# Kernel optimization log

Hardware: AMD Instinct MI355X
Metric: run time of the kernel (lower is better)

## Reference

```python
import jax, jax.numpy as jnp
import numpy as np

EPS = 1e-6
B, N, M, C, H = 4, 2048, 1024, 1024, 16
HD = C // H          # 64
HID = 4 * C          # 4096
SCALE = 1.0 / np.sqrt(HD)


def _ln(x, g, b):
    m = x.mean(-1, keepdims=True)
    v = jnp.mean((x - m) ** 2, -1, keepdims=True)
    return (x - m) * jax.lax.rsqrt(v + EPS) * g + b


def _rot(x):
    # interleaved rotate: (-x2, x1) pairs (rotate_half=False path)
    x1, x2 = x[..., ::2], x[..., 1::2]
    return jnp.stack([-x2, x1], axis=-1).reshape(x.shape)


def _apply_rope(x, emb):
    # emb: [N, 2*HD] = cat(sin, cos); x: [B,H,N,HD]
    sin, cos = jnp.split(emb, 2, axis=-1)
    return x * cos + _rot(x) * sin


def _sdpa(q, k, v):
    s = jnp.einsum('bhqd,bhkd->bhqk', q, k) * SCALE
    a = jax.nn.softmax(s, axis=-1)
    return jnp.einsum('bhqk,bhkd->bhqd', a, v)


def _forward(x, ctx, rope,
             wqkv, sa_qg, sa_qb, sa_kg, sa_kb, sa_wo, sa_bo,
             ca_wq, ca_wk, ca_wv, ca_qg, ca_qb, ca_kg, ca_kb, ca_wo, ca_bo, ca_gate,
             w1g, b1g, w1x, b1x, w2, b2, ls0, ls1, ls2):
    Bx, Nx, Cx = x.shape
    Mx = ctx.shape[1]
    # ---- self attention (fused QKV, qk-norm, RoPE) ----
    qkv = (x @ wqkv).reshape(Bx, Nx, 3, H, HD).transpose(2, 0, 3, 1, 4)  # [3,B,H,N,HD]
    q, k, v = qkv[0], qkv[1], qkv[2]
    q = _ln(q, sa_qg, sa_qb)
    k = _ln(k, sa_kg, sa_kb)
    q = _apply_rope(q, rope)
    k = _apply_rope(k, rope)
    sa = _sdpa(q, k, v).transpose(0, 2, 1, 3).reshape(Bx, Nx, Cx)
    sa = sa @ sa_wo + sa_bo
    x = ls0 * sa + x
    # ---- cross attention (GQA degenerate: n_kv_heads == n_q_heads), gated ----
    q = (x @ ca_wq).reshape(Bx, Nx, H, HD).transpose(0, 2, 1, 3)
    k = (ctx @ ca_wk).reshape(Bx, Mx, H, HD).transpose(0, 2, 1, 3)
    v = (ctx @ ca_wv).reshape(Bx, Mx, H, HD).transpose(0, 2, 1, 3)
    q = _ln(q, ca_qg, ca_qb)
    k = _ln(k, ca_kg, ca_kb)
    q = _apply_rope(q, rope)  # rope on queries only; ctx has its own positions
    ca = _sdpa(q, k, v).transpose(0, 2, 1, 3).reshape(Bx, Nx, Cx)
    ca = (ca @ ca_wo + ca_bo) * jnp.tanh(ca_gate)
    x = ls1 * ca + x
    # ---- SwiGLU FFN ----
    h = jax.nn.silu(x @ w1g + b1g) * (x @ w1x + b1x)
    f = h @ w2 + b2
    x = ls2 * f + x
    return x


def setup_inputs() -> dict:
    key = jax.random.key(0)
    ks = iter(jax.random.split(key, 32))
    rn = lambda shape, s=0.02: (jax.random.normal(next(ks), shape, jnp.float32) * s)
    inp = {
        'x': jax.random.normal(next(ks), (B, N, C), jnp.float32),
        'ctx': jax.random.normal(next(ks), (B, M, C), jnp.float32),
    }
    # rotary table: cat(sin, cos), interleaved-repeated freqs -> [N, 2*HD]
    pos = jnp.arange(N, dtype=jnp.float32)
    inv = 1.0 / (10000.0 ** (jnp.arange(0, HD, 2, dtype=jnp.float32) / HD))
    ang = pos[:, None] * inv[None, :]                      # [N, HD/2]
    sin = jnp.repeat(jnp.sin(ang), 2, axis=-1)
    cos = jnp.repeat(jnp.cos(ang), 2, axis=-1)
    inp['rope'] = jnp.concatenate([sin, cos], axis=-1)
    inp.update(
        wqkv=rn((C, 3 * C)),
        sa_qg=jnp.ones((HD,)), sa_qb=jnp.zeros((HD,)),
        sa_kg=jnp.ones((HD,)), sa_kb=jnp.zeros((HD,)),
        sa_wo=rn((C, C)), sa_bo=jnp.zeros((C,)),
        ca_wq=rn((C, C)), ca_wk=rn((C, C)), ca_wv=rn((C, C)),
        ca_qg=jnp.ones((HD,)), ca_qb=jnp.zeros((HD,)),
        ca_kg=jnp.ones((HD,)), ca_kb=jnp.zeros((HD,)),
        ca_wo=rn((C, C)), ca_bo=jnp.zeros((C,)),
        ca_gate=jnp.full((C,), 0.5, jnp.float32),
        w1g=rn((C, HID)), b1g=jnp.zeros((HID,)),
        w1x=rn((C, HID)), b1x=jnp.zeros((HID,)),
        w2=rn((HID, C)), b2=jnp.zeros((C,)),
        ls0=jnp.full((C,), 1e-5, jnp.float32),
        ls1=jnp.full((C,), 1e-5, jnp.float32),
        ls2=jnp.full((C,), 1e-5, jnp.float32),
    )
    return inp


def reference(x, ctx, rope,
              wqkv, sa_qg, sa_qb, sa_kg, sa_kb, sa_wo, sa_bo,
              ca_wq, ca_wk, ca_wv, ca_qg, ca_qb, ca_kg, ca_kb, ca_wo, ca_bo, ca_gate,
              w1g, b1g, w1x, b1x, w2, b2, ls0, ls1, ls2):
    return _forward(x, ctx, rope,
                    wqkv, sa_qg, sa_qb, sa_kg, sa_kb, sa_wo, sa_bo,
                    ca_wq, ca_wk, ca_wv, ca_qg, ca_qb, ca_kg, ca_kb, ca_wo, ca_bo, ca_gate,
                    w1g, b1g, w1x, b1x, w2, b2, ls0, ls1, ls2)
```

## Files before the change

kernel.cpp:

```cpp
#include <hip/hip_runtime.h>
#include <hip/hip_bf16.h>
#include <math.h>


typedef __attribute__((ext_vector_type(8))) short bf16x8;
typedef __attribute__((ext_vector_type(4))) short s16x4;
typedef __attribute__((ext_vector_type(4))) float f32x4;

#define DEV __device__ __forceinline__

DEV unsigned short f2us(float f) {
  __hip_bfloat16 h = __float2bfloat16(f);
  return __builtin_bit_cast(unsigned short, h);
}

DEV void gload_lds16(const void* g, void* l) {
  __builtin_amdgcn_global_load_lds((const __attribute__((address_space(1))) void*)g,
                                   (__attribute__((address_space(3))) void*)l, 16, 0, 0);
}

#define MFMA_BF16_16x16x32 __builtin_amdgcn_mfma_f32_16x16x32_bf16
#define WAITV0 asm volatile("s_waitcnt vmcnt(0)" ::: "memory")


__global__ __launch_bounds__(256) void cvt_f32_bf16(const float* __restrict__ in,
                                                    __hip_bfloat16* __restrict__ out,
                                                    long n) {
  long i = ((long)blockIdx.x * blockDim.x + threadIdx.x) * 4;
  if (i + 3 < n) {
    float4 v = *(const float4*)(in + i);
    out[i + 0] = __float2bfloat16(v.x);
    out[i + 1] = __float2bfloat16(v.y);
    out[i + 2] = __float2bfloat16(v.z);
    out[i + 3] = __float2bfloat16(v.w);
  }
}

__global__ __launch_bounds__(256) void transpose_cvt(const float* __restrict__ w,
                                                     __hip_bfloat16* __restrict__ wT,
                                                     int K, int N) {
  __shared__ float tile[32][33];
  int n0 = blockIdx.x * 32, k0 = blockIdx.y * 32;
  int tx = threadIdx.x, ty = threadIdx.y;
  #pragma unroll
  for (int i = 0; i < 32; i += 8)
    tile[ty + i][tx] = w[(long)(k0 + ty + i) * N + n0 + tx];
  __syncthreads();
  #pragma unroll
  for (int i = 0; i < 32; i += 8)
    wT[(long)(n0 + ty + i) * K + k0 + tx] = __float2bfloat16(tile[tx][ty + i]);
}

__global__ __launch_bounds__(256) void transpose_cvt_ilv(const float* __restrict__ w,
                                                         __hip_bfloat16* __restrict__ wI,
                                                         int K, int N, int ofs) {
  __shared__ float tile[32][33];
  int n0 = blockIdx.x * 32, k0 = blockIdx.y * 32;
  int tx = threadIdx.x, ty = threadIdx.y;
  #pragma unroll
  for (int i = 0; i < 32; i += 8)
    tile[ty + i][tx] = w[(long)(k0 + ty + i) * N + n0 + tx];
  __syncthreads();
  #pragma unroll
  for (int i = 0; i < 32; i += 8) {
    int j = n0 + ty + i;
    int r = 32 * (j >> 4) + (j & 15) + ofs;
    wI[(long)r * K + k0 + tx] = __float2bfloat16(tile[tx][ty + i]);
  }
}

__global__ __launch_bounds__(256) void transpose_v(const __hip_bfloat16* __restrict__ v,
                                                   long vBatch, long vRow,
                                                   __hip_bfloat16* __restrict__ vt,
                                                   int Nkv) {
  __shared__ unsigned short tile[32][36];
  int bh = blockIdx.z;
  int b = bh >> 4, h = bh & 15;
  int kv0 = blockIdx.x * 32;
  int d0 = blockIdx.y * 32;
  int tx = threadIdx.x, ty = threadIdx.y;
  const __hip_bfloat16* src = v + (long)b * vBatch + h * 64 + d0;
  #pragma unroll
  for (int i = 0; i < 32; i += 8)
    tile[ty + i][tx] = __builtin_bit_cast(unsigned short, src[(long)(kv0 + ty + i) * vRow + tx]);
  __syncthreads();
  unsigned short* dst = (unsigned short*)vt + ((long)bh * (Nkv >> 6) + (kv0 >> 6)) * 4608 + (kv0 & 32) + tx;
  #pragma unroll
  for (int i = 0; i < 32; i += 8)
    dst[(long)(d0 + ty + i) * 72] = tile[tx][ty + i];
}

__global__ __launch_bounds__(256) void ln_rope(__hip_bfloat16* __restrict__ buf,
                                               const float* __restrict__ rope,
                                               const float* __restrict__ g0,
                                               const float* __restrict__ b0,
                                               const float* __restrict__ g1,
                                               const float* __restrict__ b1,
                                               int Rows, int W,
                                               long rowStride, long whichStride,
                                               int ropeMask, long total) {
  int lane = threadIdx.x & 63;
  int wv = threadIdx.x >> 6;
  long id = (long)blockIdx.x * 4 + wv;
  if (id >= total) return;
  int which = (int)(id % W);
  long t = id / W;
  int h = (int)(t & 15); t >>= 4;
  int n = (int)(t % Rows);
  int b = (int)(t / Rows);
  __hip_bfloat16* p = buf + ((long)b * Rows + n) * rowStride + (long)which * whichStride + h * 64 + lane;
  float v = __bfloat162float(*p);
  float s = v;
  #pragma unroll
  for (int m = 32; m; m >>= 1) s += __shfl_xor(s, m);
  float mean = s * (1.f / 64.f);
  float d = v - mean;
  float q = d * d;
  #pragma unroll
  for (int m = 32; m; m >>= 1) q += __shfl_xor(q, m);
  float rstd = rsqrtf(q * (1.f / 64.f) + 1e-6f);
  const float* g = which ? g1 : g0;
  const float* bb = which ? b1 : b0;
  float xn = d * rstd * g[lane] + bb[lane];
  if ((ropeMask >> which) & 1) {
    float partner = __shfl_xor(xn, 1);
    float sn = rope[(long)n * 128 + lane];
    float cs = rope[(long)n * 128 + 64 + lane];
    xn = (lane & 1) ? (xn * cs + partner * sn) : (xn * cs - partner * sn);
  }
  *p = __float2bfloat16(xn);
}

template <int EPI>
DEV void epi_store(long idx, long col, float v,
                   float* __restrict__ out_f, __hip_bfloat16* __restrict__ out_b,
                   const float* __restrict__ bias, const float* __restrict__ scale,
                   const float* __restrict__ gate, const float* __restrict__ resid,
                   const __hip_bfloat16* __restrict__ mulin) {
  if constexpr (EPI == 0) {
    out_b[idx] = __float2bfloat16(v);
  } else if constexpr (EPI == 1) {
    float r = scale[col] * (v + bias[col]) + resid[idx];
    out_f[idx] = r;
    out_b[idx] = __float2bfloat16(r);
  } else if constexpr (EPI == 2) {
    float r = scale[col] * ((v + bias[col]) * tanhf(gate[col])) + resid[idx];
    out_f[idx] = r;
    out_b[idx] = __float2bfloat16(r);
  } else if constexpr (EPI == 3) {
    float z = v + bias[col];
    out_b[idx] = __float2bfloat16(z / (1.f + expf(-z)));
  } else if constexpr (EPI == 4) {
    float z = (v + bias[col]) * __bfloat162float(mulin[idx]);
    out_b[idx] = __float2bfloat16(z);
  } else {
    out_f[idx] = scale[col] * (v + bias[col]) + resid[idx];
  }
}

template <int EPI>
__global__ __launch_bounds__(256) void gemm128(const __hip_bfloat16* __restrict__ A,
                                               const __hip_bfloat16* __restrict__ Bt,
                                               int M, int N, int K,
                                               float* __restrict__ out_f,
                                               __hip_bfloat16* __restrict__ out_b,
                                               const float* __restrict__ bias,
                                               const float* __restrict__ scale,
                                               const float* __restrict__ gate,
                                               const float* __restrict__ resid,
                                               const __hip_bfloat16* __restrict__ mulin) {
  __shared__ unsigned short As[128 * 32];
  __shared__ unsigned short Bs[128 * 32];
  int t = threadIdx.x;
  int l = t & 63;
  int w = t >> 6;
  int wr = w >> 1, wc = w & 1;
  long bm = blockIdx.x, bn = blockIdx.y;
  const __hip_bfloat16* Ab = A + bm * 128 * (long)K;
  const __hip_bfloat16* Bb = Bt + bn * 128 * (long)K;

  f32x4 acc[4][4] = {};

  for (int k0 = 0; k0 < K; k0 += 32) {
    #pragma unroll
    for (int j = 0; j < 2; j++) {
      int c = j * 256 + t;
      int row = c >> 2;
      int ko = (c & 3) * 8;
      gload_lds16(Ab + (long)row * K + k0 + ko, &As[c * 8]);
      gload_lds16(Bb + (long)row * K + k0 + ko, &Bs[c * 8]);
    }
    __syncthreads();
    bf16x8 af[4], bfg[4];
    #pragma unroll
    for (int m = 0; m < 4; m++)
      af[m] = *(const bf16x8*)&As[(wr * 64 + m * 16 + (l & 15)) * 32 + (l >> 4) * 8];
    #pragma unroll
    for (int n = 0; n < 4; n++)
      bfg[n] = *(const bf16x8*)&Bs[(wc * 64 + n * 16 + (l & 15)) * 32 + (l >> 4) * 8];
    #pragma unroll
    for (int m = 0; m < 4; m++)
      #pragma unroll
      for (int n = 0; n < 4; n++)
        acc[m][n] = MFMA_BF16_16x16x32(af[m], bfg[n], acc[m][n], 0, 0, 0);
    __syncthreads();
  }

  #pragma unroll
  for (int m = 0; m < 4; m++)
    #pragma unroll
    for (int n = 0; n < 4; n++)
      #pragma unroll
      for (int i = 0; i < 4; i++) {
        long row = bm * 128 + wr * 64 + m * 16 + (l >> 4) * 4 + i;
        long col = bn * 128 + wc * 64 + n * 16 + (l & 15);
        epi_store<EPI>(row * (long)N + col, col, acc[m][n][i],
                       out_f, out_b, bias, scale, gate, resid, mulin);
      }
}

template <int BM, int EPI>
__global__ __launch_bounds__(512, 2) void gemm2ph(const __hip_bfloat16* __restrict__ A,
                                                  const __hip_bfloat16* __restrict__ Bt,
                                                  int M, int N, int K,
                                                  float* __restrict__ out_f,
                                                  __hip_bfloat16* __restrict__ out_b,
                                                  const float* __restrict__ bias,
                                                  const float* __restrict__ scale,
                                                  const float* __restrict__ gate,
                                                  const float* __restrict__ resid,
                                                  const __hip_bfloat16* __restrict__ mulin) {
  constexpr int MF = BM / 32;
  constexpr int WRS = BM / 2;
  constexpr int AJ = BM * 8 / 512;
  __shared__ __align__(16) unsigned short As[2][BM * 64];
  __shared__ __align__(16) unsigned short Bs[2][256 * 64];

  int t = threadIdx.x;
  int l = t & 63, w = t >> 6;
  int lo = l & 15, hi = l >> 4;
  int wr = w >> 2, wc = w & 3;
  long bm = blockIdx.x, bn = blockIdx.y;
  const __hip_bfloat16* Ab = A + bm * BM * (long)K;
  const __hip_bfloat16* Bb = Bt + bn * 256 * (long)K;
  int nt = K >> 6;

  auto stage = [&](int kt, int buf) {
    long kb = (long)kt * 64;
    #pragma unroll
    for (int j = 0; j < AJ; j++) {
      int q = j * 512 + t;
      int row = q >> 3, c = (q & 7) ^ (row & 7);
      gload_lds16(Ab + (long)row * K + kb + c * 8, &As[buf][q * 8]);
    }
    #pragma unroll
    for (int j = 0; j < 4; j++) {
      int q = j * 512 + t;
      int row = q >> 3, c = (q & 7) ^ (row & 7);
      gload_lds16(Bb + (long)row * K + kb + c * 8, &Bs[buf][q * 8]);
    }
  };

  f32x4 acc[MF][4] = {};

  stage(0, 0);
  WAITV0;
  __builtin_amdgcn_s_barrier();

  for (int kt = 0; kt < nt; ++kt) {
    int cur = kt & 1;
    if (kt + 1 < nt) stage(kt + 1, cur ^ 1);

    #pragma unroll
    for (int ks = 0; ks < 2; ks++) {
      bf16x8 bfrag[4];
      #pragma unroll
      for (int n = 0; n < 4; n++) {
        int rb = wc * 64 + n * 16 + lo;
        bfrag[n] = *(const bf16x8*)&Bs[cur][rb * 64 + (((ks << 2) | hi) ^ (rb & 7)) * 8];
      }
      #pragma unroll
      for (int mg = 0; mg < MF; mg += 4) {
        bf16x8 afrag[4];
        #pragma unroll
        for (int m = 0; m < 4; m++) {
          int ra = wr * WRS + (mg + m) * 16 + lo;
          afrag[m] = *(const bf16x8*)&As[cur][ra * 64 + (((ks << 2) | hi) ^ (ra & 7)) * 8];
        }
        __builtin_amdgcn_s_setprio(1);
        #pragma unroll
        for (int m = 0; m < 4; m++)
          #pragma unroll
          for (int n = 0; n < 4; n++)
            acc[mg + m][n] = MFMA_BF16_16x16x32(afrag[m], bfrag[n], acc[mg + m][n], 0, 0, 0);
        __builtin_amdgcn_s_setprio(0);
      }
    }

    if (kt + 1 < nt) {
      WAITV0;
      __builtin_amdgcn_s_barrier();
    }
  }

  if constexpr (EPI == 6) {
    #pragma unroll
    for (int m = 0; m < MF; m++)
      #pragma unroll
      for (int np = 0; np < 2; np++)
        #pragma unroll
        for (int i = 0; i < 4; i++) {
          long row = bm * BM + wr * WRS + m * 16 + hi * 4 + i;
          long jc = bn * 128 + wc * 32 + np * 16 + lo;
          float g = acc[m][np * 2][i] + bias[jc];
          float xv = acc[m][np * 2 + 1][i] + gate[jc];
          float hv = (g / (1.f + expf(-g))) * xv;
          out_b[row * (long)(N >> 1) + jc] = __float2bfloat16(hv);
        }
  } else {
    #pragma unroll
    for (int m = 0; m < MF; m++)
      #pragma unroll
      for (int n = 0; n < 4; n++)
        #pragma unroll
        for (int i = 0; i < 4; i++) {
          long row = bm * BM + wr * WRS + m * 16 + hi * 4 + i;
          long col = bn * 256 + wc * 64 + n * 16 + lo;
          epi_store<EPI>(row * (long)N + col, col, acc[m][n][i],
                         out_f, out_b, bias, scale, gate, resid, mulin);
        }
  }
}

__global__ __launch_bounds__(256) void attn32(const __hip_bfloat16* __restrict__ qB, long qBatch, long qRow,
                                              const __hip_bfloat16* __restrict__ kB, long kBatch, long kRow,
                                              const __hip_bfloat16* __restrict__ vt,
                                              __hip_bfloat16* __restrict__ out, int Nq, int Nkv) {
  const float SC2 = 0.125f * 1.44269504089f;
  int t = threadIdx.x;
  int l = t & 63, w = t >> 6;
  int lo = l & 15, hi = l >> 4;
  int nQC = Nq >> 7;
  int qc = blockIdx.x % nQC;
  int bh = blockIdx.x / nQC;
  int h = bh & 15, b = bh >> 4;
  int q0 = qc * 128 + w * 32;

  __shared__ unsigned short P_all[4][32 * 72];
  __shared__ unsigned short V_lds[2][64 * 72];
  unsigned short* P = P_all[w];

  bf16x8 qf[2][2];
#pragma unroll
  for (int qs = 0; qs < 2; qs++) {
    const __hip_bfloat16* qp = qB + (long)b * qBatch + (long)(q0 + qs * 16 + lo) * qRow + h * 64 + hi * 8;
    qf[qs][0] = *(const bf16x8*)qp;
    qf[qs][1] = *(const bf16x8*)(qp + 32);
  }

  float mrow[2] = {-INFINITY, -INFINITY};
  float lsum[2] = {0.f, 0.f};
  f32x4 acc[2][4] = {};
  const f32x4 fz = {0.f, 0.f, 0.f, 0.f};

  const __hip_bfloat16* kbase = kB + (long)b * kBatch + h * 64 + hi * 8;
  int nt = Nkv >> 6;
  const char* vtb = (const char*)vt + (long)bh * nt * 9216;

  auto stageV = [&](int tile, unsigned short* dstb) {
    const char* src = vtb + (long)tile * 9216;
    gload_lds16(src + t * 16, &dstb[t * 8]);
    gload_lds16(src + (t + 256) * 16, &dstb[(t + 256) * 8]);
    if (t < 64) gload_lds16(src + (t + 512) * 16, &dstb[(t + 512) * 8]);
  };
  auto loadK = [&](int tile, bf16x8 (&kg)[4][2]) {
#pragma unroll
    for (int g = 0; g < 4; g++) {
      const __hip_bfloat16* kp = kbase + (long)(tile * 64 + g * 16 + lo) * kRow;
      kg[g][0] = *(const bf16x8*)kp;
      kg[g][1] = *(const bf16x8*)(kp + 32);
    }
  };
  auto qkt = [&](bf16x8 (&kg)[4][2], f32x4 (&ST)[2][4]) {
#pragma unroll
    for (int qs = 0; qs < 2; qs++)
#pragma unroll
      for (int g = 0; g < 4; g++) {
        f32x4 s0 = MFMA_BF16_16x16x32(kg[g][0], qf[qs][0], fz, 0, 0, 0);
        ST[qs][g] = MFMA_BF16_16x16x32(kg[g][1], qf[qs][1], s0, 0, 0, 0);
      }
  };
  auto smax = [&](f32x4 (&ST)[2][4]) {
#pragma unroll
    for (int qs = 0; qs < 2; qs++) {
      float mg0 = fmaxf(fmaxf(ST[qs][0][0], ST[qs][0][1]), fmaxf(ST[qs][0][2], ST[qs][0][3]));
      float mg1 = fmaxf(fmaxf(ST[qs][1][0], ST[qs][1][1]), fmaxf(ST[qs][1][2], ST[qs][1][3]));
      float mg2 = fmaxf(fmaxf(ST[qs][2][0], ST[qs][2][1]), fmaxf(ST[qs][2][2], ST[qs][2][3]));
      float mg3 = fmaxf(fmaxf(ST[qs][3][0], ST[qs][3][1]), fmaxf(ST[qs][3][2], ST[qs][3][3]));
      float rm = fmaxf(fmaxf(mg0, mg1), fmaxf(mg2, mg3)) * SC2;
      rm = fmaxf(rm, __shfl_xor(rm, 16));
      rm = fmaxf(rm, __shfl_xor(rm, 32));
      if (!__all(rm <= mrow[qs] + 8.f)) {
        float mn = fmaxf(mrow[qs], rm);
        float scl = exp2f(mrow[qs] - mn);
        mrow[qs] = mn;
        lsum[qs] *= scl;
        float c0 = __shfl(scl, hi * 4 + 0);
        float c1 = __shfl(scl, hi * 4 + 1);
        float c2 = __shfl(scl, hi * 4 + 2);
        float c3 = __shfl(scl, hi * 4 + 3);
#pragma unroll
        for (int tt = 0; tt < 4; tt++) {
          acc[qs][tt][0] *= c0; acc[qs][tt][1] *= c1;
          acc[qs][tt][2] *= c2; acc[qs][tt][3] *= c3;
        }
      }
      float m = mrow[qs];
      float rs = 0.f;
#pragma unroll
      for (int g = 0; g < 4; g++) {
        float p0 = exp2f(fmaf(ST[qs][g][0], SC2, -m));
        float p1 = exp2f(fmaf(ST[qs][g][1], SC2, -m));
        float p2 = exp2f(fmaf(ST[qs][g][2], SC2, -m));
        float p3 = exp2f(fmaf(ST[qs][g][3], SC2, -m));
        rs += (p0 + p1) + (p2 + p3);
        s16x4 pw;
        pw[0] = (short)f2us(p0); pw[1] = (short)f2us(p1);
        pw[2] = (short)f2us(p2); pw[3] = (short)f2us(p3);
        *(s16x4*)&P[(qs * 16 + lo) * 72 + g * 16 + hi * 4] = pw;
      }
      rs += __shfl_xor(rs, 16);
      rs += __shfl_xor(rs, 32);
      lsum[qs] += rs;
    }
  };
  auto pv = [&](const unsigned short* Vb) {
    bf16x8 pf[2][2];
#pragma unroll
    for (int qs = 0; qs < 2; qs++) {
      pf[qs][0] = *(const bf16x8*)&P[(qs * 16 + lo) * 72 + hi * 8];
      pf[qs][1] = *(const bf16x8*)&P[(qs * 16 + lo) * 72 + 32 + hi * 8];
    }
#pragma unroll
    for (int tt = 0; tt < 4; tt++) {
      bf16x8 v0 = *(const bf16x8*)&Vb[(tt * 16 + lo) * 72 + hi * 8];
      bf16x8 v1 = *(const bf16x8*)&Vb[(tt * 16 + lo) * 72 + 32 + hi * 8];
#pragma unroll
      for (int qs = 0; qs < 2; qs++) {
        acc[qs][tt] = MFMA_BF16_16x16x32(pf[qs][0], v0, acc[qs][tt], 0, 0, 0);
        acc[qs][tt] = MFMA_BF16_16x16x32(pf[qs][1], v1, acc[qs][tt], 0, 0, 0);
      }
    }
  };

  bf16x8 kgA[4][2], kgB[4][2];
  stageV(0, V_lds[0]);
  loadK(0, kgA);

  for (int it = 0; it < nt; it += 2) {
    __syncthreads();
    stageV(it + 1, V_lds[1]);
    f32x4 ST0[2][4];
    qkt(kgA, ST0);
    loadK(it + 1, kgB);
    smax(ST0);
    pv(V_lds[0]);

    __syncthreads();
    if (it + 2 < nt) stageV(it + 2, V_lds[0]);
    f32x4 ST1[2][4];
    qkt(kgB, ST1);
    if (it + 2 < nt) loadK(it + 2, kgA);
    smax(ST1);
    pv(V_lds[1]);
  }

#pragma unroll
  for (int qs = 0; qs < 2; qs++) {
    float inv = 1.f / lsum[qs];
    float iv0 = __shfl(inv, hi * 4 + 0);
    float iv1 = __shfl(inv, hi * 4 + 1);
    float iv2 = __shfl(inv, hi * 4 + 2);
    float iv3 = __shfl(inv, hi * 4 + 3);
    float iv[4] = {iv0, iv1, iv2, iv3};
#pragma unroll
    for (int i = 0; i < 4; i++) {
      long row = q0 + qs * 16 + hi * 4 + i;
      __hip_bfloat16* op = out + ((long)b * Nq + row) * 1024 + h * 64 + lo;
#pragma unroll
      for (int tt = 0; tt < 4; tt++) op[tt * 16] = __float2bfloat16(acc[qs][tt][i] * iv[i]);
    }
  }
}


extern "C" void kernel_launch(void* const* d_in, const int* in_sizes, int n_in,
                              void* d_out, int out_size, void* d_ws, size_t ws_size,
                              hipStream_t stream) {
  (void)in_sizes; (void)n_in; (void)out_size; (void)ws_size;

  const float* x      = (const float*)d_in[0];
  const float* ctx    = (const float*)d_in[1];
  const float* rope   = (const float*)d_in[2];
  const float* wqkv   = (const float*)d_in[3];
  const float* sa_qg  = (const float*)d_in[4];
  const float* sa_qb  = (const float*)d_in[5];
  const float* sa_kg  = (const float*)d_in[6];
  const float* sa_kb  = (const float*)d_in[7];
  const float* sa_wo  = (const float*)d_in[8];
  const float* sa_bo  = (const float*)d_in[9];
  const float* ca_wq  = (const float*)d_in[10];
  const float* ca_wk  = (const float*)d_in[11];
  const float* ca_wv  = (const float*)d_in[12];
  const float* ca_qg  = (const float*)d_in[13];
  const float* ca_qb  = (const float*)d_in[14];
  const float* ca_kg  = (const float*)d_in[15];
  const float* ca_kb  = (const float*)d_in[16];
  const float* ca_wo  = (const float*)d_in[17];
  const float* ca_bo  = (const float*)d_in[18];
  const float* ca_gate= (const float*)d_in[19];
  const float* w1g    = (const float*)d_in[20];
  const float* b1g    = (const float*)d_in[21];
  const float* w1x    = (const float*)d_in[22];
  const float* b1x    = (const float*)d_in[23];
  const float* w2     = (const float*)d_in[24];
  const float* b2     = (const float*)d_in[25];
  const float* ls0    = (const float*)d_in[26];
  const float* ls1    = (const float*)d_in[27];
  const float* ls2    = (const float*)d_in[28];

  char* ws = (char*)d_ws;

  const long OFF_WQKVT = 0;
  const long OFF_SAWOT = 6291456;
  const long OFF_CAWQT = 8388608;
  const long OFF_CAWKT = 10485760;
  const long OFF_CAWVT = 12582912;
  const long OFF_CAWOT = 14680064;
  const long OFF_W1I   = 16777216;
  const long OFF_W2T   = 33554432;
  const long OFF_XB    = 41943040;
  const long OFF_QC    = OFF_XB;
  const long OFF_CTXB  = 58720256;
  const long OFF_QKV   = 67108864;
  const long OFF_CAO   = 67108864;
  const long OFF_X2B   = 83886080;
  const long OFF_SG    = 100663296;
  const long OFF_SAO   = 117440512;
  const long OFF_KC    = 117440512;
  const long OFF_VC    = 125829120;
  const long OFF_X1    = 134217728;
  const long OFF_X1B   = 167772160;
  const long OFF_CAVT  = OFF_X1B;
  const long OFF_X2    = 184549376;
  const long OFF_SAVT  = OFF_X2;

  auto bfp = [&](long off) { return (__hip_bfloat16*)(ws + off); };
  auto ffp = [&](long off) { return (float*)(ws + off); };

  dim3 tb32(32, 8);
  transpose_cvt<<<dim3(96, 32), tb32, 0, stream>>>(wqkv,  bfp(OFF_WQKVT), 1024, 3072);
  transpose_cvt<<<dim3(32, 32), tb32, 0, stream>>>(sa_wo, bfp(OFF_SAWOT), 1024, 1024);
  transpose_cvt<<<dim3(32, 32), tb32, 0, stream>>>(ca_wq, bfp(OFF_CAWQT), 1024, 1024);
  transpose_cvt<<<dim3(32, 32), tb32, 0, stream>>>(ca_wk, bfp(OFF_CAWKT), 1024, 1024);
  transpose_cvt<<<dim3(32, 32), tb32, 0, stream>>>(ca_wv, bfp(OFF_CAWVT), 1024, 1024);
  transpose_cvt<<<dim3(32, 32), tb32, 0, stream>>>(ca_wo, bfp(OFF_CAWOT), 1024, 1024);
  transpose_cvt_ilv<<<dim3(128, 32), tb32, 0, stream>>>(w1g, bfp(OFF_W1I), 1024, 4096, 0);
  transpose_cvt_ilv<<<dim3(128, 32), tb32, 0, stream>>>(w1x, bfp(OFF_W1I), 1024, 4096, 16);
  transpose_cvt<<<dim3(32, 128), tb32, 0, stream>>>(w2,   bfp(OFF_W2T), 4096, 1024);

  cvt_f32_bf16<<<8192, 256, 0, stream>>>(x,   bfp(OFF_XB),   8388608);
  cvt_f32_bf16<<<4096, 256, 0, stream>>>(ctx, bfp(OFF_CTXB), 4194304);

  gemm2ph<256, 0><<<dim3(32, 12), 512, 0, stream>>>(bfp(OFF_XB), bfp(OFF_WQKVT), 8192, 3072, 1024,
                                                    nullptr, bfp(OFF_QKV), nullptr, nullptr, nullptr, nullptr, nullptr);

  transpose_v<<<dim3(64, 2, 64), tb32, 0, stream>>>(bfp(OFF_QKV) + 2048, (long)2048 * 3072, 3072,
                                                    bfp(OFF_SAVT), 2048);

  ln_rope<<<65536, 256, 0, stream>>>(bfp(OFF_QKV), rope, sa_qg, sa_qb, sa_kg, sa_kb,
                                     2048, 2, 3 * 1024, 1024, 3, (long)4 * 2048 * 16 * 2);

  attn32<<<1024, 256, 0, stream>>>(bfp(OFF_QKV),        (long)2048 * 3072, 3072,
                                   bfp(OFF_QKV) + 1024, (long)2048 * 3072, 3072,
                                   bfp(OFF_SAVT), bfp(OFF_SAO), 2048, 2048);

  gemm2ph<128, 1><<<dim3(64, 4), 512, 0, stream>>>(bfp(OFF_SAO), bfp(OFF_SAWOT), 8192, 1024, 1024,
                                                   ffp(OFF_X1), bfp(OFF_X1B), sa_bo, ls0, nullptr, x, nullptr);

  gemm2ph<128, 0><<<dim3(64, 4), 512, 0, stream>>>(bfp(OFF_X1B), bfp(OFF_CAWQT), 8192, 1024, 1024,
                                                   nullptr, bfp(OFF_QC), nullptr, nullptr, nullptr, nullptr, nullptr);
  gemm128<0><<<dim3(32, 8), 256, 0, stream>>>(bfp(OFF_CTXB), bfp(OFF_CAWKT), 4096, 1024, 1024,
                                              nullptr, bfp(OFF_KC), nullptr, nullptr, nullptr, nullptr, nullptr);
  gemm128<0><<<dim3(32, 8), 256, 0, stream>>>(bfp(OFF_CTXB), bfp(OFF_CAWVT), 4096, 1024, 1024,
                                              nullptr, bfp(OFF_VC), nullptr, nullptr, nullptr, nullptr, nullptr);

  transpose_v<<<dim3(32, 2, 64), tb32, 0, stream>>>(bfp(OFF_VC), (long)1024 * 1024, 1024,
                                                    bfp(OFF_CAVT), 1024);

  ln_rope<<<32768, 256, 0, stream>>>(bfp(OFF_QC), rope, ca_qg, ca_qb, ca_qg, ca_qb,
                                     2048, 1, 1024, 0, 1, (long)4 * 2048 * 16);
  ln_rope<<<16384, 256, 0, stream>>>(bfp(OFF_KC), rope, ca_kg, ca_kb, ca_kg, ca_kb,
                                     1024, 1, 1024, 0, 0, (long)4 * 1024 * 16);

  attn32<<<1024, 256, 0, stream>>>(bfp(OFF_QC), (long)2048 * 1024, 1024,
                                   bfp(OFF_KC), (long)1024 * 1024, 1024,
                                   bfp(OFF_CAVT), bfp(OFF_CAO), 2048, 1024);

  gemm2ph<128, 2><<<dim3(64, 4), 512, 0, stream>>>(bfp(OFF_CAO), bfp(OFF_CAWOT), 8192, 1024, 1024,
                                                   ffp(OFF_X2), bfp(OFF_X2B), ca_bo, ls1, ca_gate, ffp(OFF_X1), nullptr);

  gemm2ph<256, 6><<<dim3(32, 32), 512, 0, stream>>>(bfp(OFF_X2B), bfp(OFF_W1I), 8192, 8192, 1024,
                                                    nullptr, bfp(OFF_SG), b1g, nullptr, b1x, nullptr, nullptr);

  gemm2ph<128, 5><<<dim3(64, 4), 512, 0, stream>>>(bfp(OFF_SG), bfp(OFF_W2T), 8192, 1024, 4096,
                                                   (float*)d_out, nullptr, b2, ls2, nullptr, ffp(OFF_X2), nullptr);
}
```

Before: 886.5 us.

## Fuse cross-attn K/V projections, retile QKV GEMM, prioritize MFMA in attention

Merges the two separate ctx K and V projection GEMMs into one gemm2ph launch with N=2048, relying on contiguous CAWKT/CAWVT weights. The downstream transpose, ln_rope and attention now use stride 2048 into the combined buffer. The self-attention QKV GEMM switches from BM=256 to BM=128 with twice as many blocks. The attention kernel raises wave priority around its MFMA sections with s_setprio. These target launch count, occupancy and tail effects, and MFMA issue contention, but assume the K/V weight transposes are laid out back to back.

Measured after the change: 878.3 us. No clear change (-0.9%).

```diff
diff --git a/kernel.cpp b/kernel.cpp
--- a/kernel.cpp
+++ b/kernel.cpp
@@ -156,67 +156,6 @@
   } else {
     out_f[idx] = scale[col] * (v + bias[col]) + resid[idx];
   }
-}
-
-template <int EPI>
-__global__ __launch_bounds__(256) void gemm128(const __hip_bfloat16* __restrict__ A,
-                                               const __hip_bfloat16* __restrict__ Bt,
-                                               int M, int N, int K,
-                                               float* __restrict__ out_f,
-                                               __hip_bfloat16* __restrict__ out_b,
-                                               const float* __restrict__ bias,
-                                               const float* __restrict__ scale,
-                                               const float* __restrict__ gate,
-                                               const float* __restrict__ resid,
-                                               const __hip_bfloat16* __restrict__ mulin) {
-  __shared__ unsigned short As[128 * 32];
-  __shared__ unsigned short Bs[128 * 32];
-  int t = threadIdx.x;
-  int l = t & 63;
-  int w = t >> 6;
-  int wr = w >> 1, wc = w & 1;
-  long bm = blockIdx.x, bn = blockIdx.y;
-  const __hip_bfloat16* Ab = A + bm * 128 * (long)K;
-  const __hip_bfloat16* Bb = Bt + bn * 128 * (long)K;
-
-  f32x4 acc[4][4] = {};
-
-  for (int k0 = 0; k0 < K; k0 += 32) {
-    #pragma unroll
-    for (int j = 0; j < 2; j++) {
-      int c = j * 256 + t;
-      int row = c >> 2;
-      int ko = (c & 3) * 8;
-      gload_lds16(Ab + (long)row * K + k0 + ko, &As[c * 8]);
-      gload_lds16(Bb + (long)row * K + k0 + ko, &Bs[c * 8]);
-    }
-    __syncthreads();
-    bf16x8 af[4], bfg[4];
-    #pragma unroll
-    for (int m = 0; m < 4; m++)
-      af[m] = *(const bf16x8*)&As[(wr * 64 + m * 16 + (l & 15)) * 32 + (l >> 4) * 8];
-    #pragma unroll
-    for (int n = 0; n < 4; n++)
-      bfg[n] = *(const bf16x8*)&Bs[(wc * 64 + n * 16 + (l & 15)) * 32 + (l >> 4) * 8];
-    #pragma unroll
-    for (int m = 0; m < 4; m++)
-      #pragma unroll
-      for (int n = 0; n < 4; n++)
-        acc[m][n] = MFMA_BF16_16x16x32(af[m], bfg[n], acc[m][n], 0, 0, 0);
-    __syncthreads();
-  }
-
-  #pragma unroll
-  for (int m = 0; m < 4; m++)
-    #pragma unroll
-    for (int n = 0; n < 4; n++)
-      #pragma unroll
-      for (int i = 0; i < 4; i++) {
-        long row = bm * 128 + wr * 64 + m * 16 + (l >> 4) * 4 + i;
-        long col = bn * 128 + wc * 64 + n * 16 + (l & 15);
-        epi_store<EPI>(row * (long)N + col, col, acc[m][n][i],
-                       out_f, out_b, bias, scale, gate, resid, mulin);
-      }
 }
 
 template <int BM, int EPI>
@@ -382,6 +321,7 @@
     }
   };
   auto qkt = [&](bf16x8 (&kg)[4][2], f32x4 (&ST)[2][4]) {
+    __builtin_amdgcn_s_setprio(1);
 #pragma unroll
     for (int qs = 0; qs < 2; qs++)
 #pragma unroll
@@ -389,6 +329,7 @@
         f32x4 s0 = MFMA_BF16_16x16x32(kg[g][0], qf[qs][0], fz, 0, 0, 0);
         ST[qs][g] = MFMA_BF16_16x16x32(kg[g][1], qf[qs][1], s0, 0, 0, 0);
       }
+    __builtin_amdgcn_s_setprio(0);
   };
   auto smax = [&](f32x4 (&ST)[2][4]) {
 #pragma unroll
@@ -441,6 +382,7 @@
       pf[qs][0] = *(const bf16x8*)&P[(qs * 16 + lo) * 72 + hi * 8];
       pf[qs][1] = *(const bf16x8*)&P[(qs * 16 + lo) * 72 + 32 + hi * 8];
     }
+    __builtin_amdgcn_s_setprio(1);
 #pragma unroll
     for (int tt = 0; tt < 4; tt++) {
       bf16x8 v0 = *(const bf16x8*)&Vb[(tt * 16 + lo) * 72 + hi * 8];
@@ -451,6 +393,7 @@
         acc[qs][tt] = MFMA_BF16_16x16x32(pf[qs][1], v1, acc[qs][tt], 0, 0, 0);
       }
     }
+    __builtin_amdgcn_s_setprio(0);
   };
 
   bf16x8 kgA[4][2], kgB[4][2];
@@ -547,8 +490,7 @@
   const long OFF_X2B   = 83886080;
   const long OFF_SG    = 100663296;
   const long OFF_SAO   = 117440512;
-  const long OFF_KC    = 117440512;
-  const long OFF_VC    = 125829120;
+  const long OFF_KVC   = 117440512;
   const long OFF_X1    = 134217728;
   const long OFF_X1B   = 167772160;
   const long OFF_CAVT  = OFF_X1B;
@@ -572,7 +514,7 @@
   cvt_f32_bf16<<<8192, 256, 0, stream>>>(x,   bfp(OFF_XB),   8388608);
   cvt_f32_bf16<<<4096, 256, 0, stream>>>(ctx, bfp(OFF_CTXB), 4194304);
 
-  gemm2ph<256, 0><<<dim3(32, 12), 512, 0, stream>>>(bfp(OFF_XB), bfp(OFF_WQKVT), 8192, 3072, 1024,
+  gemm2ph<128, 0><<<dim3(64, 12), 512, 0, stream>>>(bfp(OFF_XB), bfp(OFF_WQKVT), 8192, 3072, 1024,
                                                     nullptr, bfp(OFF_QKV), nullptr, nullptr, nullptr, nullptr, nullptr);
 
   transpose_v<<<dim3(64, 2, 64), tb32, 0, stream>>>(bfp(OFF_QKV) + 2048, (long)2048 * 3072, 3072,
@@ -590,21 +532,19 @@
 
   gemm2ph<128, 0><<<dim3(64, 4), 512, 0, stream>>>(bfp(OFF_X1B), bfp(OFF_CAWQT), 8192, 1024, 1024,
                                                    nullptr, bfp(OFF_QC), nullptr, nullptr, nullptr, nullptr, nullptr);
-  gemm128<0><<<dim3(32, 8), 256, 0, stream>>>(bfp(OFF_CTXB), bfp(OFF_CAWKT), 4096, 1024, 1024,
-                                              nullptr, bfp(OFF_KC), nullptr, nullptr, nullptr, nullptr, nullptr);
-  gemm128<0><<<dim3(32, 8), 256, 0, stream>>>(bfp(OFF_CTXB), bfp(OFF_CAWVT), 4096, 1024, 1024,
-                                              nullptr, bfp(OFF_VC), nullptr, nullptr, nullptr, nullptr, nullptr);
-
-  transpose_v<<<dim3(32, 2, 64), tb32, 0, stream>>>(bfp(OFF_VC), (long)1024 * 1024, 1024,
+  gemm2ph<128, 0><<<dim3(32, 8), 512, 0, stream>>>(bfp(OFF_CTXB), bfp(OFF_CAWKT), 4096, 2048, 1024,
+                                                   nullptr, bfp(OFF_KVC), nullptr, nullptr, nullptr, nullptr, nullptr);
+
+  transpose_v<<<dim3(32, 2, 64), tb32, 0, stream>>>(bfp(OFF_KVC) + 1024, (long)1024 * 2048, 2048,
                                                     bfp(OFF_CAVT), 1024);
 
   ln_rope<<<32768, 256, 0, stream>>>(bfp(OFF_QC), rope, ca_qg, ca_qb, ca_qg, ca_qb,
                                      2048, 1, 1024, 0, 1, (long)4 * 2048 * 16);
-  ln_rope<<<16384, 256, 0, stream>>>(bfp(OFF_KC), rope, ca_kg, ca_kb, ca_kg, ca_kb,
-                                     1024, 1, 1024, 0, 0, (long)4 * 1024 * 16);
+  ln_rope<<<16384, 256, 0, stream>>>(bfp(OFF_KVC), rope, ca_kg, ca_kb, ca_kg, ca_kb,
+                                     1024, 1, 2048, 0, 0, (long)4 * 1024 * 16);
 
   attn32<<<1024, 256, 0, stream>>>(bfp(OFF_QC), (long)2048 * 1024, 1024,
-                                   bfp(OFF_KC), (long)1024 * 1024, 1024,
+                                   bfp(OFF_KVC), (long)1024 * 2048, 2048,
                                    bfp(OFF_CAVT), bfp(OFF_CAO), 2048, 1024);
 
   gemm2ph<128, 2><<<dim3(64, 4), 512, 0, stream>>>(bfp(OFF_CAO), bfp(OFF_CAWOT), 8192, 1024, 1024,
```
